# Optimization experiments

Measured on AMD Instinct MI355X. Metric: run time of the kernel, lower is better.

The kernel has to match this reference:

```python
import jax, jax.numpy as jnp
import numpy as np

N = 25000   # nodes
E = 400000  # edges (avg degree 16)
H = 128     # hidden_dim
L = 4       # n_layers
TE = 8      # type_emb_dim
SD = 5      # scalar_dim


def setup_inputs() -> dict:
    key = jax.random.key(0)
    ks = jax.random.split(key, 30)
    w = lambda k, shape: (jax.random.normal(k, shape, dtype=jnp.float32) * 0.1)
    inp = {
        'node_pos': jax.random.normal(ks[0], (N, 3), dtype=jnp.float32),
        'node_scalar': jax.random.normal(ks[1], (N, SD), dtype=jnp.float32),
        'type_ids': jax.random.randint(ks[2], (N,), 0, 5),
        'edge_index': jax.random.randint(ks[3], (2, E), 0, N),
        'emb': w(ks[4], (5, TE)),
        'W_in': w(ks[5], (SD + TE, H)), 'b_in': jnp.zeros((H,), jnp.float32),
        # edge_mlp: Linear(2H+1,H) SiLU Linear(H,H) SiLU Linear(H,H), stacked over L layers
        'eW1': w(ks[6], (L, 2 * H + 1, H)), 'eb1': jnp.zeros((L, H), jnp.float32),
        'eW2': w(ks[7], (L, H, H)), 'eb2': jnp.zeros((L, H), jnp.float32),
        'eW3': w(ks[8], (L, H, H)), 'eb3': jnp.zeros((L, H), jnp.float32),
        # coord_mlp: Linear(H,H) SiLU Linear(H,1)
        'cW1': w(ks[9], (L, H, H)), 'cb1': jnp.zeros((L, H), jnp.float32),
        'cW2': w(ks[10], (L, H, 1)), 'cb2': jnp.zeros((L, 1), jnp.float32),
        # node_mlp: Linear(2H,H) SiLU Linear(H,H) SiLU Linear(H,H)
        'nW1': w(ks[11], (L, 2 * H, H)), 'nb1': jnp.zeros((L, H), jnp.float32),
        'nW2': w(ks[12], (L, H, H)), 'nb2': jnp.zeros((L, H), jnp.float32),
        'nW3': w(ks[13], (L, H, H)), 'nb3': jnp.zeros((L, H), jnp.float32),
        # readout
        'W_ro': w(ks[14], (H, H)), 'b_ro': jnp.zeros((H,), jnp.float32),
    }
    return inp


def _geo_encoder(node_pos, node_scalar, type_ids, edge_index,
                 emb, W_in, b_in,
                 eW1, eb1, eW2, eb2, eW3, eb3,
                 cW1, cb1, cW2, cb2,
                 nW1, nb1, nW2, nb2, nW3, nb3,
                 W_ro, b_ro):
    n_nodes = node_pos.shape[0]
    silu = jax.nn.silu
    tids = jnp.clip(type_ids, 0, emb.shape[0] - 1)
    feats = jnp.concatenate([node_scalar, emb[tids]], axis=-1)  # [N, SD+TE]
    h = feats @ W_in + b_in                                     # [N, H]
    x = node_pos                                                # [N, 3]
    src, dst = edge_index[0], edge_index[1]
    for l in range(eW1.shape[0]):
        rel = x[src] - x[dst]                                   # [E, 3]
        d2 = jnp.sum(rel * rel, axis=-1, keepdims=True)         # [E, 1]
        e_in = jnp.concatenate([h[src], h[dst], d2], axis=-1)   # [E, 2H+1]
        m = silu(e_in @ eW1[l] + eb1[l])
        m = silu(m @ eW2[l] + eb2[l])
        m = m @ eW3[l] + eb3[l]                                 # [E, H]
        m_aggr = jax.ops.segment_sum(m, src, num_segments=n_nodes)  # [N, H]
        coord_coef = jnp.tanh(silu(m @ cW1[l] + cb1[l]) @ cW2[l] + cb2[l])  # [E, 1]
        delta_x = jax.ops.segment_sum(rel * coord_coef, src, num_segments=n_nodes)
        x = x + delta_x
        n_in = jnp.concatenate([h, m_aggr], axis=-1)            # [N, 2H]
        hh = silu(n_in @ nW1[l] + nb1[l])
        hh = silu(hh @ nW2[l] + nb2[l])
        h = h + (hh @ nW3[l] + nb3[l])
    z_nodes = h @ W_ro + b_ro                                   # [N, H]
    z_global = jnp.mean(z_nodes, axis=0)                        # [H]
    return z_global, z_nodes


def reference(node_pos, node_scalar, type_ids, edge_index,
              emb, W_in, b_in,
              eW1, eb1, eW2, eb2, eW3, eb3,
              cW1, cb1, cW2, cb2,
              nW1, nb1, nW2, nb2, nW3, nb3,
              W_ro, b_ro):
    return _geo_encoder(node_pos, node_scalar, type_ids, edge_index,
                        emb, W_in, b_in,
                        eW1, eb1, eW2, eb2, eW3, eb3,
                        cW1, cb1, cW2, cb2,
                        nW1, nb1, nW2, nb2, nW3, nb3,
                        W_ro, b_ro)
```

## Files before the change

### kernel.cpp

```cpp
#include <hip/hip_runtime.h>
#include <math.h>

#define H 128
#define LDSTR 68

__device__ __forceinline__ float silu_f(float v) {
    return v / (1.0f + __expf(-v));
}

__device__ __forceinline__ void gemm_b(const float (*__restrict__ buf)[LDSTR],
                                       const float* __restrict__ W,
                                       int f2, int ew,
                                       float acc0[16], float acc1[16]) {
#pragma unroll 4
    for (int k = 0; k < H; ++k) {
        const float2 w  = *(const float2*)&W[(size_t)k * H + f2];
        const float4 a0 = *(const float4*)&buf[k][ew + 0];
        const float4 a1 = *(const float4*)&buf[k][ew + 4];
        const float4 a2 = *(const float4*)&buf[k][ew + 8];
        const float4 a3 = *(const float4*)&buf[k][ew + 12];
        const float av[16] = {a0.x, a0.y, a0.z, a0.w, a1.x, a1.y, a1.z, a1.w,
                              a2.x, a2.y, a2.z, a2.w, a3.x, a3.y, a3.z, a3.w};
#pragma unroll
        for (int i = 0; i < 16; ++i) {
            acc0[i] = fmaf(w.x, av[i], acc0[i]);
            acc1[i] = fmaf(w.y, av[i], acc1[i]);
        }
    }
}

template <bool DO_SILU>
__device__ __forceinline__ void writeback(float (*__restrict__ buf)[LDSTR],
                                          int f2, int ew,
                                          const float acc0[16], const float acc1[16]) {
#pragma unroll
    for (int t = 0; t < 4; ++t) {
        float4 v0, v1;
        v0.x = acc0[4 * t + 0]; v0.y = acc0[4 * t + 1]; v0.z = acc0[4 * t + 2]; v0.w = acc0[4 * t + 3];
        v1.x = acc1[4 * t + 0]; v1.y = acc1[4 * t + 1]; v1.z = acc1[4 * t + 2]; v1.w = acc1[4 * t + 3];
        if (DO_SILU) {
            v0.x = silu_f(v0.x); v0.y = silu_f(v0.y); v0.z = silu_f(v0.z); v0.w = silu_f(v0.w);
            v1.x = silu_f(v1.x); v1.y = silu_f(v1.y); v1.z = silu_f(v1.z); v1.w = silu_f(v1.w);
        }
        *(float4*)&buf[f2 + 0][ew + 4 * t] = v0;
        *(float4*)&buf[f2 + 1][ew + 4 * t] = v1;
    }
}

__device__ __forceinline__ void stage_rows(const float* __restrict__ rowp, int q, int lane,
                                           float (*__restrict__ buf)[LDSTR]) {
#pragma unroll
    for (int c = 0; c < 8; ++c) {
        const float4 v = *(const float4*)(rowp + 4 * c);
        const int f = q * 32 + 4 * c;
        buf[f + 0][lane] = v.x;
        buf[f + 1][lane] = v.y;
        buf[f + 2][lane] = v.z;
        buf[f + 3][lane] = v.w;
    }
}

__device__ __forceinline__ void prefetch_row(const float* __restrict__ rowp, float4 pre[8]) {
#pragma unroll
    for (int c = 0; c < 8; ++c) pre[c] = *(const float4*)(rowp + 4 * c);
}

__device__ __forceinline__ void store_pre(const float4 pre[8], int q, int lane,
                                          float (*__restrict__ buf)[LDSTR]) {
#pragma unroll
    for (int c = 0; c < 8; ++c) {
        const int f = q * 32 + 4 * c;
        buf[f + 0][lane] = pre[c].x;
        buf[f + 1][lane] = pre[c].y;
        buf[f + 2][lane] = pre[c].z;
        buf[f + 3][lane] = pre[c].w;
    }
}

__global__ void __launch_bounds__(256)
input_kernel(const float* __restrict__ node_scalar, const int* __restrict__ type_ids,
             const float* __restrict__ emb, const float* __restrict__ W_in,
             const float* __restrict__ b_in, float* __restrict__ hout,
             int NN, int ntypes)
{
    const int idx = blockIdx.x * 256 + threadIdx.x;
    if (idx >= NN * H) return;
    const int n = idx >> 7;
    const int f = idx & (H - 1);
    int t = type_ids[n];
    t = t < 0 ? 0 : (t >= ntypes ? ntypes - 1 : t);
    float s = b_in[f];
#pragma unroll
    for (int k = 0; k < 5; ++k) s = fmaf(node_scalar[n * 5 + k], W_in[k * H + f], s);
#pragma unroll
    for (int k = 0; k < 8; ++k) s = fmaf(emb[t * 8 + k], W_in[(5 + k) * H + f], s);
    hout[idx] = s;
}

__global__ void __launch_bounds__(256, 4)
edge_kernel(const float* __restrict__ x, const float* __restrict__ h,
            const int* __restrict__ src, const int* __restrict__ dst,
            const float* __restrict__ eW1, const float* __restrict__ eb1,
            const float* __restrict__ eW2, const float* __restrict__ eb2,
            const float* __restrict__ eW3, const float* __restrict__ eb3,
            const float* __restrict__ cW1, const float* __restrict__ cb1,
            const float* __restrict__ cW2, const float* __restrict__ cb2,
            float* __restrict__ m_aggr, float* __restrict__ dxv,
            int E)
{
    __shared__ float buf[H][LDSTR];
    __shared__ float d2s[64];
    __shared__ float relx[64], rely[64], relz[64];
    __shared__ int   ssrc[64], sdst[64];
    __shared__ int   evalid[64];

    const int tid  = threadIdx.x;
    const int lane = tid & 63;
    const int q    = tid >> 6;
    const int f2   = lane * 2;
    const int ew   = q * 16;
    const int e0   = blockIdx.x * 64;

    if (tid < 64) {
        int e = e0 + tid;
        int v = (e < E) ? 1 : 0;
        if (!v) e = E - 1;
        evalid[tid] = v;
        const int s = src[e], d = dst[e];
        ssrc[tid] = s; sdst[tid] = d;
        const float rx = x[3 * s + 0] - x[3 * d + 0];
        const float ry = x[3 * s + 1] - x[3 * d + 1];
        const float rz = x[3 * s + 2] - x[3 * d + 2];
        relx[tid] = rx; rely[tid] = ry; relz[tid] = rz;
        d2s[tid] = rx * rx + ry * ry + rz * rz;
    }
    __syncthreads();

    float4 pre[8];
    prefetch_row(h + (size_t)sdst[lane] * H + q * 32, pre);
    stage_rows(h + (size_t)ssrc[lane] * H + q * 32, q, lane, buf);
    __syncthreads();

    float acc0[16], acc1[16];
    {
        const float2 bv = *(const float2*)&eb1[f2];
        const float2 wd = *(const float2*)&eW1[(size_t)256 * H + f2];
#pragma unroll
        for (int i = 0; i < 16; ++i) {
            const float d2 = d2s[ew + i];
            acc0[i] = fmaf(d2, wd.x, bv.x);
            acc1[i] = fmaf(d2, wd.y, bv.y);
        }
    }
    gemm_b(buf, eW1, f2, ew, acc0, acc1);
    __syncthreads();
    store_pre(pre, q, lane, buf);
    __syncthreads();
    gemm_b(buf, eW1 + (size_t)128 * H, f2, ew, acc0, acc1);
    __syncthreads();

    writeback<true>(buf, f2, ew, acc0, acc1);
    __syncthreads();

    {
        const float2 bv = *(const float2*)&eb2[f2];
#pragma unroll
        for (int i = 0; i < 16; ++i) { acc0[i] = bv.x; acc1[i] = bv.y; }
    }
    gemm_b(buf, eW2, f2, ew, acc0, acc1);
    __syncthreads();
    writeback<true>(buf, f2, ew, acc0, acc1);
    __syncthreads();

    {
        const float2 bv = *(const float2*)&eb3[f2];
#pragma unroll
        for (int i = 0; i < 16; ++i) { acc0[i] = bv.x; acc1[i] = bv.y; }
    }
    gemm_b(buf, eW3, f2, ew, acc0, acc1);

#pragma unroll
    for (int i = 0; i < 16; ++i) {
        const int e = ew + i;
        if (evalid[e]) {
            float* dp = &m_aggr[(size_t)ssrc[e] * H + f2];
            atomicAdd(dp + 0, acc0[i]);
            atomicAdd(dp + 1, acc1[i]);
        }
    }
    __syncthreads();
    writeback<false>(buf, f2, ew, acc0, acc1);
    __syncthreads();

    {
        const float2 bv = *(const float2*)&cb1[f2];
#pragma unroll
        for (int i = 0; i < 16; ++i) { acc0[i] = bv.x; acc1[i] = bv.y; }
    }
    gemm_b(buf, cW1, f2, ew, acc0, acc1);

    {
        const float2 c2 = *(const float2*)&cW2[f2];
        float p[16];
#pragma unroll
        for (int i = 0; i < 16; ++i)
            p[i] = fmaf(silu_f(acc0[i]), c2.x, silu_f(acc1[i]) * c2.y);
#pragma unroll
        for (int msk = 1; msk < 64; msk <<= 1)
#pragma unroll
            for (int i = 0; i < 16; ++i)
                p[i] += __shfl_xor(p[i], msk);
        float myp = 0.f;
#pragma unroll
        for (int i = 0; i < 16; ++i) myp = (lane == i) ? p[i] : myp;
        if (lane < 16) {
            const int e = ew + lane;
            if (evalid[e]) {
                const float coef = tanhf(myp + cb2[0]);
                float* dp = &dxv[(size_t)ssrc[e] * 3];
                atomicAdd(dp + 0, relx[e] * coef);
                atomicAdd(dp + 1, rely[e] * coef);
                atomicAdd(dp + 2, relz[e] * coef);
            }
        }
    }
}

__global__ void __launch_bounds__(256, 4)
node_kernel(float* __restrict__ x, const float* __restrict__ dxv,
            float* __restrict__ h, const float* __restrict__ m_aggr,
            const float* __restrict__ nW1, const float* __restrict__ nb1,
            const float* __restrict__ nW2, const float* __restrict__ nb2,
            const float* __restrict__ nW3, const float* __restrict__ nb3,
            int NN)
{
    __shared__ float buf[H][LDSTR];

    const int tid  = threadIdx.x;
    const int lane = tid & 63;
    const int q    = tid >> 6;
    const int f2   = lane * 2;
    const int ew   = q * 16;
    const int n0   = blockIdx.x * 64;

    const int nl = n0 + lane;
    const int nc = (nl < NN) ? nl : NN - 1;

    if (tid < 192) {
        const int nn = n0 + tid / 3;
        if (nn < NN) {
            const int c = tid % 3;
            x[(size_t)nn * 3 + c] += dxv[(size_t)nn * 3 + c];
        }
    }

    float4 pre[8];
    prefetch_row(m_aggr + (size_t)nc * H + q * 32, pre);
    stage_rows(h + (size_t)nc * H + q * 32, q, lane, buf);
    __syncthreads();

    float acc0[16], acc1[16];
    {
        const float2 bv = *(const float2*)&nb1[f2];
#pragma unroll
        for (int i = 0; i < 16; ++i) { acc0[i] = bv.x; acc1[i] = bv.y; }
    }
    gemm_b(buf, nW1, f2, ew, acc0, acc1);
    __syncthreads();
    store_pre(pre, q, lane, buf);
    __syncthreads();
    gemm_b(buf, nW1 + (size_t)128 * H, f2, ew, acc0, acc1);
    __syncthreads();

    writeback<true>(buf, f2, ew, acc0, acc1);
    __syncthreads();

    {
        const float2 bv = *(const float2*)&nb2[f2];
#pragma unroll
        for (int i = 0; i < 16; ++i) { acc0[i] = bv.x; acc1[i] = bv.y; }
    }
    gemm_b(buf, nW2, f2, ew, acc0, acc1);
    __syncthreads();
    writeback<true>(buf, f2, ew, acc0, acc1);
    __syncthreads();

    {
        const float2 bv = *(const float2*)&nb3[f2];
#pragma unroll
        for (int i = 0; i < 16; ++i) { acc0[i] = bv.x; acc1[i] = bv.y; }
    }
    gemm_b(buf, nW3, f2, ew, acc0, acc1);

#pragma unroll
    for (int i = 0; i < 16; ++i) {
        const int n = n0 + ew + i;
        if (n < NN) {
            float2* hp = (float2*)&h[(size_t)n * H + f2];
            float2 v = *hp;
            v.x += acc0[i]; v.y += acc1[i];
            *hp = v;
        }
    }
}

__global__ void __launch_bounds__(256, 4)
readout_kernel(const float* __restrict__ h, const float* __restrict__ W_ro,
               const float* __restrict__ b_ro, float* __restrict__ out, int NN)
{
    __shared__ float buf[H][LDSTR];
    __shared__ float sred[4][H];

    const int tid  = threadIdx.x;
    const int lane = tid & 63;
    const int q    = tid >> 6;
    const int f2   = lane * 2;
    const int ew   = q * 16;
    const int n0   = blockIdx.x * 64;

    const int nl = n0 + lane;
    const int nc = (nl < NN) ? nl : NN - 1;

    stage_rows(h + (size_t)nc * H + q * 32, q, lane, buf);
    __syncthreads();

    float acc0[16], acc1[16];
    {
        const float2 bv = *(const float2*)&b_ro[f2];
#pragma unroll
        for (int i = 0; i < 16; ++i) { acc0[i] = bv.x; acc1[i] = bv.y; }
    }
    gemm_b(buf, W_ro, f2, ew, acc0, acc1);

    float* zn = out + H;
    float s0 = 0.f, s1 = 0.f;
#pragma unroll
    for (int i = 0; i < 16; ++i) {
        const int n = n0 + ew + i;
        if (n < NN) {
            float2* zp = (float2*)&zn[(size_t)n * H + f2];
            float2 v; v.x = acc0[i]; v.y = acc1[i];
            *zp = v;
            s0 += acc0[i]; s1 += acc1[i];
        }
    }
    sred[q][f2 + 0] = s0;
    sred[q][f2 + 1] = s1;
    __syncthreads();
    if (tid < H) {
        const float inv = 1.0f / (float)NN;
        const float v = (sred[0][tid] + sred[1][tid] + sred[2][tid] + sred[3][tid]) * inv;
        atomicAdd(&out[tid], v);
    }
}

extern "C" void kernel_launch(void* const* d_in, const int* in_sizes, int n_in,
                              void* d_out, int out_size, void* d_ws, size_t ws_size,
                              hipStream_t stream) {
    const float* node_pos    = (const float*)d_in[0];
    const float* node_scalar = (const float*)d_in[1];
    const int*   type_ids    = (const int*)d_in[2];
    const int*   edge_index  = (const int*)d_in[3];
    const float* emb         = (const float*)d_in[4];
    const float* W_in        = (const float*)d_in[5];
    const float* b_in        = (const float*)d_in[6];
    const float* eW1 = (const float*)d_in[7];
    const float* eb1 = (const float*)d_in[8];
    const float* eW2 = (const float*)d_in[9];
    const float* eb2 = (const float*)d_in[10];
    const float* eW3 = (const float*)d_in[11];
    const float* eb3 = (const float*)d_in[12];
    const float* cW1 = (const float*)d_in[13];
    const float* cb1 = (const float*)d_in[14];
    const float* cW2 = (const float*)d_in[15];
    const float* cb2 = (const float*)d_in[16];
    const float* nW1 = (const float*)d_in[17];
    const float* nb1 = (const float*)d_in[18];
    const float* nW2 = (const float*)d_in[19];
    const float* nb2 = (const float*)d_in[20];
    const float* nW3 = (const float*)d_in[21];
    const float* nb3 = (const float*)d_in[22];
    const float* W_ro = (const float*)d_in[23];
    const float* b_ro = (const float*)d_in[24];

    const int NN = in_sizes[0] / 3;
    const int E  = in_sizes[3] / 2;
    const int Lc = in_sizes[7] / ((2 * H + 1) * H);
    const int ntypes = in_sizes[4] / 8;

    const int* srcp = edge_index;
    const int* dstp = edge_index + E;

    float* hbuf = (float*)d_out + H;

    float* ws     = (float*)d_ws;
    float* m_aggr = ws;
    float* xb     = ws + (size_t)NN * H;
    float* dxb    = xb + (size_t)NN * 3;

    hipMemcpyAsync(xb, node_pos, sizeof(float) * 3 * (size_t)NN,
                   hipMemcpyDeviceToDevice, stream);
    input_kernel<<<dim3((NN * H + 255) / 256), dim3(256), 0, stream>>>(
        node_scalar, type_ids, emb, W_in, b_in, hbuf, NN, ntypes);

    for (int l = 0; l < Lc; ++l) {
        hipMemsetAsync(m_aggr, 0, sizeof(float) * (size_t)NN * H, stream);
        hipMemsetAsync(dxb, 0, sizeof(float) * (size_t)NN * 3, stream);
        edge_kernel<<<dim3((E + 63) / 64), dim3(256), 0, stream>>>(
            xb, hbuf, srcp, dstp,
            eW1 + (size_t)l * (2 * H + 1) * H, eb1 + (size_t)l * H,
            eW2 + (size_t)l * H * H,           eb2 + (size_t)l * H,
            eW3 + (size_t)l * H * H,           eb3 + (size_t)l * H,
            cW1 + (size_t)l * H * H,           cb1 + (size_t)l * H,
            cW2 + (size_t)l * H,               cb2 + l,
            m_aggr, dxb, E);
        node_kernel<<<dim3((NN + 63) / 64), dim3(256), 0, stream>>>(
            xb, dxb, hbuf, m_aggr,
            nW1 + (size_t)l * 2 * H * H, nb1 + (size_t)l * H,
            nW2 + (size_t)l * H * H,     nb2 + (size_t)l * H,
            nW3 + (size_t)l * H * H,     nb3 + (size_t)l * H, NN);
    }

    hipMemsetAsync(d_out, 0, sizeof(float) * H, stream);
    readout_kernel<<<dim3((NN + 63) / 64), dim3(256), 0, stream>>>(
        hbuf, W_ro, b_ro, (float*)d_out, NN);
}
```

Measured before the change: 4.110 ms.

## Precompute per-node eW1 projections and fold eW3 into coord MLP weights

The first edge-MLP layer is split so the h[src] and h[dst] contributions are computed once per node in a projection kernel, leaving each edge with only a gather, add and SiLU. A prep kernel also folds eW3 into cW1 (W_ec = eW3·cW1, c_ec = eb3·cW1 + cb1), so the coordinate MLP runs directly on the pre-eW3 activations and skips one shared-memory writeback and barrier per tile. Together these remove roughly two of the five 128x128 per-edge GEMMs. In exchange the change needs a larger workspace (N x 256 projection buffer), adds gather traffic for the projections, and slightly changes floating-point rounding. It falls back to the old kernel when the workspace is too small.

```diff
diff --git a/kernel.cpp b/kernel.cpp
--- a/kernel.cpp
+++ b/kernel.cpp
@@ -95,6 +95,206 @@
 #pragma unroll
     for (int k = 0; k < 8; ++k) s = fmaf(emb[t * 8 + k], W_in[(5 + k) * H + f], s);
     hout[idx] = s;
+}
+
+__global__ void __launch_bounds__(256)
+prep_kernel(const float* __restrict__ eW3, const float* __restrict__ eb3,
+            const float* __restrict__ cW1, const float* __restrict__ cb1,
+            float* __restrict__ W_ec, float* __restrict__ c_ec)
+{
+    const int l = blockIdx.x;
+    const float* A  = eW3 + (size_t)l * H * H;
+    const float* Bw = cW1 + (size_t)l * H * H;
+    float* O = W_ec + (size_t)l * H * H;
+    const int tid = threadIdx.x;
+    const int k  = tid >> 1;
+    const int jh = (tid & 1) * 64;
+    float acc[64];
+#pragma unroll
+    for (int j = 0; j < 64; ++j) acc[j] = 0.f;
+    for (int t = 0; t < H; ++t) {
+        const float a = A[k * H + t];
+        const float* br = Bw + t * H + jh;
+#pragma unroll
+        for (int j = 0; j < 64; ++j) acc[j] = fmaf(a, br[j], acc[j]);
+    }
+#pragma unroll
+    for (int j = 0; j < 64; ++j) O[k * H + jh + j] = acc[j];
+
+    if (tid < H) {
+        const float* b3 = eb3 + (size_t)l * H;
+        float s = cb1[(size_t)l * H + tid];
+        for (int t = 0; t < H; ++t) s = fmaf(b3[t], Bw[t * H + tid], s);
+        c_ec[(size_t)l * H + tid] = s;
+    }
+}
+
+__global__ void __launch_bounds__(256, 4)
+proj_kernel(const float* __restrict__ h, const float* __restrict__ eW1,
+            const float* __restrict__ eb1, float* __restrict__ P, int NN)
+{
+    __shared__ float buf[H][LDSTR];
+    const int tid  = threadIdx.x;
+    const int lane = tid & 63;
+    const int q    = tid >> 6;
+    const int f2   = lane * 2;
+    const int ew   = q * 16;
+    const int n0   = blockIdx.x * 64;
+
+    const int nl = n0 + lane;
+    const int nc = (nl < NN) ? nl : NN - 1;
+    stage_rows(h + (size_t)nc * H + q * 32, q, lane, buf);
+    __syncthreads();
+
+    float acc0[16], acc1[16];
+    {
+        const float2 bv = *(const float2*)&eb1[f2];
+#pragma unroll
+        for (int i = 0; i < 16; ++i) { acc0[i] = bv.x; acc1[i] = bv.y; }
+    }
+    gemm_b(buf, eW1, f2, ew, acc0, acc1);
+#pragma unroll
+    for (int i = 0; i < 16; ++i) {
+        const int n = n0 + ew + i;
+        if (n < NN) {
+            float2 v; v.x = acc0[i]; v.y = acc1[i];
+            *(float2*)&P[(size_t)n * 256 + f2] = v;
+        }
+    }
+#pragma unroll
+    for (int i = 0; i < 16; ++i) { acc0[i] = 0.f; acc1[i] = 0.f; }
+    gemm_b(buf, eW1 + (size_t)128 * H, f2, ew, acc0, acc1);
+#pragma unroll
+    for (int i = 0; i < 16; ++i) {
+        const int n = n0 + ew + i;
+        if (n < NN) {
+            float2 v; v.x = acc0[i]; v.y = acc1[i];
+            *(float2*)&P[(size_t)n * 256 + 128 + f2] = v;
+        }
+    }
+}
+
+__global__ void __launch_bounds__(256, 4)
+edge_kernel_pre(const float* __restrict__ x, const float* __restrict__ P,
+                const int* __restrict__ src, const int* __restrict__ dst,
+                const float* __restrict__ eW1,
+                const float* __restrict__ eW2, const float* __restrict__ eb2,
+                const float* __restrict__ eW3, const float* __restrict__ eb3,
+                const float* __restrict__ W_ec, const float* __restrict__ c_ec,
+                const float* __restrict__ cW2, const float* __restrict__ cb2,
+                float* __restrict__ m_aggr, float* __restrict__ dxv,
+                int E)
+{
+    __shared__ float buf[H][LDSTR];
+    __shared__ float relx[64], rely[64], relz[64];
+    __shared__ int   ssrc[64];
+    __shared__ int   evalid[64];
+
+    const int tid  = threadIdx.x;
+    const int lane = tid & 63;
+    const int q    = tid >> 6;
+    const int f2   = lane * 2;
+    const int ew   = q * 16;
+    const int e0   = blockIdx.x * 64;
+
+    int e = e0 + lane;
+    const bool ev = (e < E);
+    if (!ev) e = E - 1;
+    const int s = src[e], d = dst[e];
+    const float rx = x[3 * s + 0] - x[3 * d + 0];
+    const float ry = x[3 * s + 1] - x[3 * d + 1];
+    const float rz = x[3 * s + 2] - x[3 * d + 2];
+    const float d2 = rx * rx + ry * ry + rz * rz;
+    if (q == 0) {
+        ssrc[lane] = s; evalid[lane] = ev ? 1 : 0;
+        relx[lane] = rx; rely[lane] = ry; relz[lane] = rz;
+    }
+
+    {
+        const float* p1  = P + (size_t)s * 256 + q * 32;
+        const float* p2  = P + (size_t)d * 256 + 128 + q * 32;
+        const float* w2r = eW1 + (size_t)256 * H + q * 32;
+#pragma unroll
+        for (int hh = 0; hh < 2; ++hh) {
+            float4 a[4], b[4], w[4];
+#pragma unroll
+            for (int c = 0; c < 4; ++c) {
+                a[c] = *(const float4*)(p1 + 16 * hh + 4 * c);
+                b[c] = *(const float4*)(p2 + 16 * hh + 4 * c);
+                w[c] = *(const float4*)(w2r + 16 * hh + 4 * c);
+            }
+#pragma unroll
+            for (int c = 0; c < 4; ++c) {
+                const int f = q * 32 + 16 * hh + 4 * c;
+                buf[f + 0][lane] = silu_f(fmaf(d2, w[c].x, a[c].x + b[c].x));
+                buf[f + 1][lane] = silu_f(fmaf(d2, w[c].y, a[c].y + b[c].y));
+                buf[f + 2][lane] = silu_f(fmaf(d2, w[c].z, a[c].z + b[c].z));
+                buf[f + 3][lane] = silu_f(fmaf(d2, w[c].w, a[c].w + b[c].w));
+            }
+        }
+    }
+    __syncthreads();
+
+    float acc0[16], acc1[16];
+    {
+        const float2 bv = *(const float2*)&eb2[f2];
+#pragma unroll
+        for (int i = 0; i < 16; ++i) { acc0[i] = bv.x; acc1[i] = bv.y; }
+    }
+    gemm_b(buf, eW2, f2, ew, acc0, acc1);
+    __syncthreads();
+    writeback<true>(buf, f2, ew, acc0, acc1);
+    __syncthreads();
+
+    {
+        const float2 bv = *(const float2*)&eb3[f2];
+#pragma unroll
+        for (int i = 0; i < 16; ++i) { acc0[i] = bv.x; acc1[i] = bv.y; }
+    }
+    gemm_b(buf, eW3, f2, ew, acc0, acc1);
+
+#pragma unroll
+    for (int i = 0; i < 16; ++i) {
+        const int ee = ew + i;
+        if (evalid[ee]) {
+            float* dp = &m_aggr[(size_t)ssrc[ee] * H + f2];
+            atomicAdd(dp + 0, acc0[i]);
+            atomicAdd(dp + 1, acc1[i]);
+        }
+    }
+
+    {
+        const float2 bv = *(const float2*)&c_ec[f2];
+#pragma unroll
+        for (int i = 0; i < 16; ++i) { acc0[i] = bv.x; acc1[i] = bv.y; }
+    }
+    gemm_b(buf, W_ec, f2, ew, acc0, acc1);
+
+    {
+        const float2 c2 = *(const float2*)&cW2[f2];
+        float p[16];
+#pragma unroll
+        for (int i = 0; i < 16; ++i)
+            p[i] = fmaf(silu_f(acc0[i]), c2.x, silu_f(acc1[i]) * c2.y);
+#pragma unroll
+        for (int msk = 1; msk < 64; msk <<= 1)
+#pragma unroll
+            for (int i = 0; i < 16; ++i)
+                p[i] += __shfl_xor(p[i], msk);
+        float myp = 0.f;
+#pragma unroll
+        for (int i = 0; i < 16; ++i) myp = (lane == i) ? p[i] : myp;
+        if (lane < 16) {
+            const int ee = ew + lane;
+            if (evalid[ee]) {
+                const float coef = tanhf(myp + cb2[0]);
+                float* dp = &dxv[(size_t)ssrc[ee] * 3];
+                atomicAdd(dp + 0, relx[ee] * coef);
+                atomicAdd(dp + 1, rely[ee] * coef);
+                atomicAdd(dp + 2, relz[ee] * coef);
+            }
+        }
+    }
 }
 
 __global__ void __launch_bounds__(256, 4)
@@ -181,9 +381,9 @@
 
 #pragma unroll
     for (int i = 0; i < 16; ++i) {
-        const int e = ew + i;
-        if (evalid[e]) {
-            float* dp = &m_aggr[(size_t)ssrc[e] * H + f2];
+        const int e2 = ew + i;
+        if (evalid[e2]) {
+            float* dp = &m_aggr[(size_t)ssrc[e2] * H + f2];
             atomicAdd(dp + 0, acc0[i]);
             atomicAdd(dp + 1, acc1[i]);
         }
@@ -214,13 +414,13 @@
 #pragma unroll
         for (int i = 0; i < 16; ++i) myp = (lane == i) ? p[i] : myp;
         if (lane < 16) {
-            const int e = ew + lane;
-            if (evalid[e]) {
+            const int e2 = ew + lane;
+            if (evalid[e2]) {
                 const float coef = tanhf(myp + cb2[0]);
-                float* dp = &dxv[(size_t)ssrc[e] * 3];
-                atomicAdd(dp + 0, relx[e] * coef);
-                atomicAdd(dp + 1, rely[e] * coef);
-                atomicAdd(dp + 2, relz[e] * coef);
+                float* dp = &dxv[(size_t)ssrc[e2] * 3];
+                atomicAdd(dp + 0, relx[e2] * coef);
+                atomicAdd(dp + 1, rely[e2] * coef);
+                atomicAdd(dp + 2, relz[e2] * coef);
             }
         }
     }
@@ -338,9 +538,8 @@
     for (int i = 0; i < 16; ++i) {
         const int n = n0 + ew + i;
         if (n < NN) {
-            float2* zp = (float2*)&zn[(size_t)n * H + f2];
             float2 v; v.x = acc0[i]; v.y = acc1[i];
-            *zp = v;
+            *(float2*)&zn[(size_t)n * H + f2] = v;
             s0 += acc0[i]; s1 += acc1[i];
         }
     }
@@ -393,27 +592,62 @@
 
     float* hbuf = (float*)d_out + H;
 
-    float* ws     = (float*)d_ws;
-    float* m_aggr = ws;
-    float* xb     = ws + (size_t)NN * H;
-    float* dxb    = xb + (size_t)NN * 3;
+    const size_t fl_P  = (size_t)NN * 256;
+    const size_t fl_ma = (size_t)NN * H;
+    const size_t fl_x  = (size_t)NN * 3;
+    const size_t fl_We = (size_t)Lc * H * H;
+    const size_t fl_ce = (size_t)Lc * H;
+    const size_t need  = (fl_P + fl_ma + 2 * fl_x + fl_We + fl_ce) * sizeof(float);
+    const bool use_proj = (ws_size >= need);
+
+    float* ws = (float*)d_ws;
+    float *P, *m_aggr, *xb, *dxb, *W_ec, *c_ec;
+    if (use_proj) {
+        P      = ws;
+        m_aggr = P + fl_P;
+        xb     = m_aggr + fl_ma;
+        dxb    = xb + fl_x;
+        W_ec   = dxb + fl_x;
+        c_ec   = W_ec + fl_We;
+    } else {
+        P = W_ec = c_ec = nullptr;
+        m_aggr = ws;
+        xb     = m_aggr + fl_ma;
+        dxb    = xb + fl_x;
+    }
 
     hipMemcpyAsync(xb, node_pos, sizeof(float) * 3 * (size_t)NN,
                    hipMemcpyDeviceToDevice, stream);
     input_kernel<<<dim3((NN * H + 255) / 256), dim3(256), 0, stream>>>(
         node_scalar, type_ids, emb, W_in, b_in, hbuf, NN, ntypes);
 
+    if (use_proj)
+        prep_kernel<<<dim3(Lc), dim3(256), 0, stream>>>(eW3, eb3, cW1, cb1, W_ec, c_ec);
+
     for (int l = 0; l < Lc; ++l) {
         hipMemsetAsync(m_aggr, 0, sizeof(float) * (size_t)NN * H, stream);
         hipMemsetAsync(dxb, 0, sizeof(float) * (size_t)NN * 3, stream);
-        edge_kernel<<<dim3((E + 63) / 64), dim3(256), 0, stream>>>(
-            xb, hbuf, srcp, dstp,
-            eW1 + (size_t)l * (2 * H + 1) * H, eb1 + (size_t)l * H,
-            eW2 + (size_t)l * H * H,           eb2 + (size_t)l * H,
-            eW3 + (size_t)l * H * H,           eb3 + (size_t)l * H,
-            cW1 + (size_t)l * H * H,           cb1 + (size_t)l * H,
-            cW2 + (size_t)l * H,               cb2 + l,
-            m_aggr, dxb, E);
+        if (use_proj) {
+            proj_kernel<<<dim3((NN + 63) / 64), dim3(256), 0, stream>>>(
+                hbuf, eW1 + (size_t)l * (2 * H + 1) * H, eb1 + (size_t)l * H, P, NN);
+            edge_kernel_pre<<<dim3((E + 63) / 64), dim3(256), 0, stream>>>(
+                xb, P, srcp, dstp,
+                eW1 + (size_t)l * (2 * H + 1) * H,
+                eW2 + (size_t)l * H * H, eb2 + (size_t)l * H,
+                eW3 + (size_t)l * H * H, eb3 + (size_t)l * H,
+                W_ec + (size_t)l * H * H, c_ec + (size_t)l * H,
+                cW2 + (size_t)l * H, cb2 + l,
+                m_aggr, dxb, E);
+        } else {
+            edge_kernel<<<dim3((E + 63) / 64), dim3(256), 0, stream>>>(
+                xb, hbuf, srcp, dstp,
+                eW1 + (size_t)l * (2 * H + 1) * H, eb1 + (size_t)l * H,
+                eW2 + (size_t)l * H * H,           eb2 + (size_t)l * H,
+                eW3 + (size_t)l * H * H,           eb3 + (size_t)l * H,
+                cW1 + (size_t)l * H * H,           cb1 + (size_t)l * H,
+                cW2 + (size_t)l * H,               cb2 + l,
+                m_aggr, dxb, E);
+        }
         node_kernel<<<dim3((NN + 63) / 64), dim3(256), 0, stream>>>(
             xb, dxb, hbuf, m_aggr,
             nW1 + (size_t)l * 2 * H * H, nb1 + (size_t)l * H,
```

New measurement: 3.353 ms. 18.4% less time.
